# Kernel tuning notes

Hardware: AMD Instinct MI355X
Metric: run time of the kernel (lower is better)

Reference implementation:

```python
import jax, jax.numpy as jnp
import numpy as np

NODES, NFEAT = 128, 256


def setup_inputs() -> dict:
    key = jax.random.key(0)
    k1, k2, k3, k4, k5, k6 = jax.random.split(key, 6)
    B = 512
    x = jax.random.normal(k1, (B, NODES, NFEAT), dtype=jnp.float32)
    adj = jax.random.uniform(k2, (B, NODES, NODES), dtype=jnp.float32)
    # GraphConvolution(nfeat, nfeat): weight [nfeat, nfeat], bias [nfeat]
    s = 1.0 / np.sqrt(NFEAT)
    gcn_w = jax.random.uniform(k3, (NFEAT, NFEAT), minval=-s, maxval=s, dtype=jnp.float32)
    gcn_b = jax.random.uniform(k4, (NFEAT,), minval=-s, maxval=s, dtype=jnp.float32)
    # fc: Linear(nfeat*nodes, nfeat), torch layout [out, in]
    s2 = 1.0 / np.sqrt(NFEAT * NODES)
    fc_w = jax.random.uniform(k5, (NFEAT, NFEAT * NODES), minval=-s2, maxval=s2, dtype=jnp.float32)
    fc_b = jax.random.uniform(k6, (NFEAT,), minval=-s2, maxval=s2, dtype=jnp.float32)
    return {"x": x, "adj": adj, "gcn_w": gcn_w, "gcn_b": gcn_b, "fc_w": fc_w, "fc_b": fc_b}


def reference(x, adj, gcn_w, gcn_b, fc_w, fc_b):
    B = x.shape[0]
    # Per-sample loop GCN fused as batched matmuls:
    # support = X @ W ; out = A @ support + b
    support = jnp.einsum('bnf,fg->bng', x, gcn_w)          # [B, nodes, nfeat]
    mid = jnp.einsum('bnm,bmg->bng', adj, support) + gcn_b  # [B, nodes, nfeat]
    # cat along dim0 then reshape(-1, nfeat*nodes) == per-graph flatten
    flat = mid.reshape(B, NODES * NFEAT)
    output = flat @ fc_w.T + fc_b                           # [B, nfeat]
    useful_input = x[:, 0, :]                               # [B, nfeat]
    return (output, useful_input, output)
```

## Files before the change

### kernel.cpp

```cpp
#include <hip/hip_runtime.h>

#define NODES 128
#define NFEAT 256
#define BATCH 512
#define KTOT  (NODES * NFEAT)
#define SPLIT 128
#define KCH   (KTOT / SPLIT)

typedef __bf16 bf16_t;
typedef bf16_t bf16x8 __attribute__((ext_vector_type(8)));
typedef float  f32x4  __attribute__((ext_vector_type(4)));

#define BK    32
#define LDK   40
#define BK2   64
#define LDK2  72
#define LDM   136
#define TILE  128

__device__ __forceinline__ bf16x8 cvt8(const float4 a, const float4 b) {
    bf16x8 t;
    t[0] = (bf16_t)a.x; t[1] = (bf16_t)a.y; t[2] = (bf16_t)a.z; t[3] = (bf16_t)a.w;
    t[4] = (bf16_t)b.x; t[5] = (bf16_t)b.y; t[6] = (bf16_t)b.z; t[7] = (bf16_t)b.w;
    return t;
}

struct XT { float4 v[4]; };
__device__ __forceinline__ void xload(const float* __restrict__ src, int ld, int k0,
                                      int tid, XT& t) {
#pragma unroll
    for (int i = 0; i < 2; i++) {
        int f = tid + i * 256, r = f >> 2, c = f & 3;
        t.v[2 * i]     = *(const float4*)(src + (size_t)r * ld + k0 + c * 8);
        t.v[2 * i + 1] = *(const float4*)(src + (size_t)r * ld + k0 + c * 8 + 4);
    }
}
__device__ __forceinline__ void xstore(bf16_t* __restrict__ dst, int tid, const XT& t) {
#pragma unroll
    for (int i = 0; i < 2; i++) {
        int f = tid + i * 256, r = f >> 2, c = f & 3;
        *(bf16x8*)(dst + r * LDK + c * 8) = cvt8(t.v[2 * i], t.v[2 * i + 1]);
    }
}

struct XT2 { float4 v[8]; };
__device__ __forceinline__ void xload2(const float* __restrict__ src, int ld, int k0,
                                       int tid, XT2& t) {
#pragma unroll
    for (int i = 0; i < 4; i++) {
        int f = tid + i * 256, r = f >> 3, c = f & 7;
        t.v[2 * i]     = *(const float4*)(src + (size_t)r * ld + k0 + c * 8);
        t.v[2 * i + 1] = *(const float4*)(src + (size_t)r * ld + k0 + c * 8 + 4);
    }
}
__device__ __forceinline__ void xstore2(bf16_t* __restrict__ dst, int tid, const XT2& t) {
#pragma unroll
    for (int i = 0; i < 4; i++) {
        int f = tid + i * 256, r = f >> 3, c = f & 7;
        *(bf16x8*)(dst + r * LDK2 + c * 8) = cvt8(t.v[2 * i], t.v[2 * i + 1]);
    }
}

struct AT2 { bf16x8 v[4]; };
__device__ __forceinline__ void aload2(const bf16_t* __restrict__ src, int ld, int k0,
                                       int tid, AT2& t) {
#pragma unroll
    for (int i = 0; i < 4; i++) {
        int f = tid + i * 256, r = f >> 3, c = f & 7;
        t.v[i] = *(const bf16x8*)(src + (size_t)r * ld + k0 + c * 8);
    }
}
__device__ __forceinline__ void astore2(bf16_t* __restrict__ dst, int tid, const AT2& t) {
#pragma unroll
    for (int i = 0; i < 4; i++) {
        int f = tid + i * 256, r = f >> 3, c = f & 7;
        *(bf16x8*)(dst + r * LDK2 + c * 8) = t.v[i];
    }
}

__global__ __launch_bounds__(256)
void k_wt(const float* __restrict__ w, bf16_t* __restrict__ wT) {
    const int g0 = blockIdx.x * 4;
    const int k  = threadIdx.x;
    const float4 v = *(const float4*)(w + (size_t)k * NFEAT + g0);
    wT[(size_t)(g0 + 0) * NFEAT + k] = (bf16_t)v.x;
    wT[(size_t)(g0 + 1) * NFEAT + k] = (bf16_t)v.y;
    wT[(size_t)(g0 + 2) * NFEAT + k] = (bf16_t)v.z;
    wT[(size_t)(g0 + 3) * NFEAT + k] = (bf16_t)v.w;
}

__global__ __launch_bounds__(256)
void k_init(const float* __restrict__ fc_b, const float* __restrict__ x,
            float* __restrict__ out) {
    const int g = blockIdx.x * 256 + threadIdx.x;
    const int o = g & (NFEAT - 1), b = g >> 8;
    out[g] = fc_b[o];
    out[BATCH * NFEAT + g] = x[(size_t)b * NODES * NFEAT + o];
}

__global__ __launch_bounds__(256)
void k_fin(float* __restrict__ out) {
    const int g = blockIdx.x * 256 + threadIdx.x;
    out[2 * BATCH * NFEAT + g] = out[g];
}

__global__ __launch_bounds__(256, 3)
void k_fused12(const float* __restrict__ x, const float* __restrict__ adj,
               const bf16_t* __restrict__ wT, const float* __restrict__ gcn_b,
               bf16_t* __restrict__ mid) {
    __shared__ __align__(16) bf16_t As[TILE * LDK];
    __shared__ __align__(16) bf16_t Sb[TILE * LDM];
    const int n0  = blockIdx.x * TILE;
    const int b   = blockIdx.y;
    const int tid = threadIdx.x;
    const int lane = tid & 63, w = tid >> 6, wm = w & 1, wn = w >> 1;
    const int l15 = lane & 15, q = lane >> 4;
    const float* xb   = x   + (size_t)b * NODES * NFEAT;
    const float* adjb = adj + (size_t)b * NODES * NODES;

    const bf16_t* wrow[4];
#pragma unroll
    for (int j = 0; j < 4; j++)
        wrow[j] = wT + (size_t)(n0 + wn * 64 + j * 16 + l15) * NFEAT + q * 8;

    f32x4 acc[4][4] = {};
    {
        XT r0, rn, r2;
        xload(xb, NFEAT, 0, tid, r0);
        xload(xb, NFEAT, BK, tid, rn);
        bf16x8 bcur[4], bnxt[4];
#pragma unroll
        for (int j = 0; j < 4; j++) bcur[j] = *(const bf16x8*)(wrow[j]);
        xstore(As, tid, r0);
        __syncthreads();
        for (int k0 = 0; k0 < NFEAT; k0 += BK) {
            const bool in1 = (k0 + BK)  < NFEAT;
            const bool in2 = (k0 + 2*BK) < NFEAT;
            if (in2) xload(xb, NFEAT, k0 + 2*BK, tid, r2);
            const int knc = in1 ? k0 + BK : 0;
#pragma unroll
            for (int j = 0; j < 4; j++) bnxt[j] = *(const bf16x8*)(wrow[j] + knc);
            bf16x8 a[4];
#pragma unroll
            for (int i = 0; i < 4; i++)
                a[i] = *(const bf16x8*)(As + (wm * 64 + i * 16 + l15) * LDK + q * 8);
#pragma unroll
            for (int i = 0; i < 4; i++)
#pragma unroll
                for (int j = 0; j < 4; j++)
                    acc[i][j] = __builtin_amdgcn_mfma_f32_16x16x32_bf16(a[i], bcur[j], acc[i][j], 0, 0, 0);
            __syncthreads();
            if (in1) xstore(As, tid, rn);
            rn = r2;
#pragma unroll
            for (int j = 0; j < 4; j++) bcur[j] = bnxt[j];
            __syncthreads();
        }
    }

    XT a0, a1, a2;
    xload(adjb, NODES, 0, tid, a0);
    xload(adjb, NODES, BK, tid, a1);
#pragma unroll
    for (int i = 0; i < 4; i++)
#pragma unroll
        for (int j = 0; j < 4; j++)
#pragma unroll
            for (int r = 0; r < 4; r++) {
                int m = wm * 64 + i * 16 + q * 4 + r;
                int g = wn * 64 + j * 16 + l15;
                Sb[g * LDM + m] = (bf16_t)acc[i][j][r];
            }
    __syncthreads();
    xstore(As, tid, a0);
    __syncthreads();

    f32x4 acc2[4][4] = {};
    for (int k0 = 0; k0 < NODES; k0 += BK) {
        const bool in1 = (k0 + BK)   < NODES;
        const bool in2 = (k0 + 2*BK) < NODES;
        if (in2) xload(adjb, NODES, k0 + 2*BK, tid, a2);
        bf16x8 a[4], bb[4];
#pragma unroll
        for (int i = 0; i < 4; i++)
            a[i] = *(const bf16x8*)(As + (wm * 64 + i * 16 + l15) * LDK + q * 8);
#pragma unroll
        for (int j = 0; j < 4; j++)
            bb[j] = *(const bf16x8*)(Sb + (wn * 64 + j * 16 + l15) * LDM + k0 + q * 8);
#pragma unroll
        for (int i = 0; i < 4; i++)
#pragma unroll
            for (int j = 0; j < 4; j++)
                acc2[i][j] = __builtin_amdgcn_mfma_f32_16x16x32_bf16(a[i], bb[j], acc2[i][j], 0, 0, 0);
        __syncthreads();
        if (in1) xstore(As, tid, a1);
        a1 = a2;
        __syncthreads();
    }
    bf16_t* outb = mid + (size_t)b * NODES * NFEAT;
#pragma unroll
    for (int j = 0; j < 4; j++) {
        int g = n0 + wn * 64 + j * 16 + l15;
        float bias = gcn_b[g];
#pragma unroll
        for (int i = 0; i < 4; i++)
#pragma unroll
            for (int r = 0; r < 4; r++) {
                int node = wm * 64 + i * 16 + q * 4 + r;
                outb[(size_t)node * NFEAT + g] = (bf16_t)(acc2[i][j][r] + bias);
            }
    }
}

__global__ __launch_bounds__(256, 3)
void k_out(const bf16_t* __restrict__ flat, const float* __restrict__ fcw,
           float* __restrict__ out) {
    __shared__ __align__(16) bf16_t As[TILE * LDK2];
    __shared__ __align__(16) bf16_t Bs[TILE * LDK2];
    const int m0 = blockIdx.x * TILE;
    const int n0 = blockIdx.y * TILE;
    const int kb = blockIdx.z * KCH, kend = kb + KCH;
    const int tid = threadIdx.x;
    const int lane = tid & 63, w = tid >> 6, wm = w & 1, wn = w >> 1;
    const int l15 = lane & 15, q = lane >> 4;
    f32x4 acc[4][4] = {};
    const bf16_t* fa = flat + (size_t)m0 * KTOT;
    const float*  fb = fcw + (size_t)n0 * KTOT;

    AT2 at; aload2(fa, KTOT, kb, tid, at);
    XT2 bt; xload2(fb, KTOT, kb, tid, bt);
    astore2(As, tid, at);
    xstore2(Bs, tid, bt);
    __syncthreads();
    for (int k0 = kb; k0 < kend; k0 += BK2) {
        const int kn = k0 + BK2;
        const bool in = kn < kend;
        AT2 an; XT2 bn;
        if (in) { aload2(fa, KTOT, kn, tid, an); xload2(fb, KTOT, kn, tid, bn); }
#pragma unroll
        for (int kk = 0; kk < BK2; kk += BK) {
            bf16x8 a[4], bbf[4];
#pragma unroll
            for (int i = 0; i < 4; i++)
                a[i] = *(const bf16x8*)(As + (wm * 64 + i * 16 + l15) * LDK2 + kk + q * 8);
#pragma unroll
            for (int j = 0; j < 4; j++)
                bbf[j] = *(const bf16x8*)(Bs + (wn * 64 + j * 16 + l15) * LDK2 + kk + q * 8);
#pragma unroll
            for (int i = 0; i < 4; i++)
#pragma unroll
                for (int j = 0; j < 4; j++)
                    acc[i][j] = __builtin_amdgcn_mfma_f32_16x16x32_bf16(a[i], bbf[j], acc[i][j], 0, 0, 0);
        }
        __syncthreads();
        if (in) { astore2(As, tid, an); xstore2(Bs, tid, bn); }
        __syncthreads();
    }
#pragma unroll
    for (int i = 0; i < 4; i++)
#pragma unroll
        for (int j = 0; j < 4; j++)
#pragma unroll
            for (int r = 0; r < 4; r++) {
                int bt_ = m0 + wm * 64 + i * 16 + q * 4 + r;
                int o   = n0 + wn * 64 + j * 16 + l15;
                atomicAdd(&out[(size_t)bt_ * NFEAT + o], acc[i][j][r]);
            }
}

extern "C" void kernel_launch(void* const* d_in, const int* in_sizes, int n_in,
                              void* d_out, int out_size, void* d_ws, size_t ws_size,
                              hipStream_t stream) {
    const float* x     = (const float*)d_in[0];
    const float* adj   = (const float*)d_in[1];
    const float* gcn_w = (const float*)d_in[2];
    const float* gcn_b = (const float*)d_in[3];
    const float* fc_w  = (const float*)d_in[4];
    const float* fc_b  = (const float*)d_in[5];
    float* out = (float*)d_out;

    bf16_t* wT  = (bf16_t*)d_ws;
    bf16_t* mid = (bf16_t*)((char*)d_ws + 131072);

    k_wt     <<<dim3(64), dim3(256), 0, stream>>>(gcn_w, wT);
    k_init   <<<dim3(BATCH), dim3(256), 0, stream>>>(fc_b, x, out);
    k_fused12<<<dim3(2, BATCH), dim3(256), 0, stream>>>(x, adj, wT, gcn_b, mid);
    k_out    <<<dim3(4, 2, SPLIT), dim3(256), 0, stream>>>(mid, fc_w, out);
    k_fin    <<<dim3(BATCH), dim3(256), 0, stream>>>(out);
}
```

Baseline: 238.9 us.

## Replace split-K atomics with bf16 partials plus reduce kernel; lighter barriers

The split-K output GEMM now writes bf16 partial tiles to workspace instead of float atomics into the output. A new reduce kernel sums them, adds the bias, and writes all three outputs, which removes the init and finish kernels. The split factor is halved to 64, and __syncthreads is replaced by an inline s_waitcnt lgkmcnt(0) plus s_barrier that skips waiting on outstanding global loads. Rounding partials to bf16 adds accumulation error, and the reduce pass adds extra memory traffic.

Measured after the change: 203.7 us. 14.7% less time.

```diff
diff --git a/kernel.cpp b/kernel.cpp
--- a/kernel.cpp
+++ b/kernel.cpp
@@ -4,7 +4,7 @@
 #define NFEAT 256
 #define BATCH 512
 #define KTOT  (NODES * NFEAT)
-#define SPLIT 128
+#define SPLIT 64
 #define KCH   (KTOT / SPLIT)
 
 typedef __bf16 bf16_t;
@@ -17,6 +17,10 @@
 #define LDK2  72
 #define LDM   136
 #define TILE  128
+
+__device__ __forceinline__ void bar() {
+    asm volatile("s_waitcnt lgkmcnt(0)\n\ts_barrier" ::: "memory");
+}
 
 __device__ __forceinline__ bf16x8 cvt8(const float4 a, const float4 b) {
     bf16x8 t;
@@ -87,21 +91,6 @@
     wT[(size_t)(g0 + 1) * NFEAT + k] = (bf16_t)v.y;
     wT[(size_t)(g0 + 2) * NFEAT + k] = (bf16_t)v.z;
     wT[(size_t)(g0 + 3) * NFEAT + k] = (bf16_t)v.w;
-}
-
-__global__ __launch_bounds__(256)
-void k_init(const float* __restrict__ fc_b, const float* __restrict__ x,
-            float* __restrict__ out) {
-    const int g = blockIdx.x * 256 + threadIdx.x;
-    const int o = g & (NFEAT - 1), b = g >> 8;
-    out[g] = fc_b[o];
-    out[BATCH * NFEAT + g] = x[(size_t)b * NODES * NFEAT + o];
-}
-
-__global__ __launch_bounds__(256)
-void k_fin(float* __restrict__ out) {
-    const int g = blockIdx.x * 256 + threadIdx.x;
-    out[2 * BATCH * NFEAT + g] = out[g];
 }
 
 __global__ __launch_bounds__(256, 3)
@@ -132,9 +121,9 @@
 #pragma unroll
         for (int j = 0; j < 4; j++) bcur[j] = *(const bf16x8*)(wrow[j]);
         xstore(As, tid, r0);
-        __syncthreads();
+        bar();
         for (int k0 = 0; k0 < NFEAT; k0 += BK) {
-            const bool in1 = (k0 + BK)  < NFEAT;
+            const bool in1 = (k0 + BK)   < NFEAT;
             const bool in2 = (k0 + 2*BK) < NFEAT;
             if (in2) xload(xb, NFEAT, k0 + 2*BK, tid, r2);
             const int knc = in1 ? k0 + BK : 0;
@@ -149,12 +138,12 @@
 #pragma unroll
                 for (int j = 0; j < 4; j++)
                     acc[i][j] = __builtin_amdgcn_mfma_f32_16x16x32_bf16(a[i], bcur[j], acc[i][j], 0, 0, 0);
-            __syncthreads();
+            bar();
             if (in1) xstore(As, tid, rn);
             rn = r2;
 #pragma unroll
             for (int j = 0; j < 4; j++) bcur[j] = bnxt[j];
-            __syncthreads();
+            bar();
         }
     }
 
@@ -171,9 +160,9 @@
                 int g = wn * 64 + j * 16 + l15;
                 Sb[g * LDM + m] = (bf16_t)acc[i][j][r];
             }
-    __syncthreads();
+    bar();
     xstore(As, tid, a0);
-    __syncthreads();
+    bar();
 
     f32x4 acc2[4][4] = {};
     for (int k0 = 0; k0 < NODES; k0 += BK) {
@@ -192,10 +181,10 @@
 #pragma unroll
             for (int j = 0; j < 4; j++)
                 acc2[i][j] = __builtin_amdgcn_mfma_f32_16x16x32_bf16(a[i], bb[j], acc2[i][j], 0, 0, 0);
-        __syncthreads();
+        bar();
         if (in1) xstore(As, tid, a1);
         a1 = a2;
-        __syncthreads();
+        bar();
     }
     bf16_t* outb = mid + (size_t)b * NODES * NFEAT;
 #pragma unroll
@@ -214,7 +203,7 @@
 
 __global__ __launch_bounds__(256, 3)
 void k_out(const bf16_t* __restrict__ flat, const float* __restrict__ fcw,
-           float* __restrict__ out) {
+           bf16_t* __restrict__ part) {
     __shared__ __align__(16) bf16_t As[TILE * LDK2];
     __shared__ __align__(16) bf16_t Bs[TILE * LDK2];
     const int m0 = blockIdx.x * TILE;
@@ -231,7 +220,7 @@
     XT2 bt; xload2(fb, KTOT, kb, tid, bt);
     astore2(As, tid, at);
     xstore2(Bs, tid, bt);
-    __syncthreads();
+    bar();
     for (int k0 = kb; k0 < kend; k0 += BK2) {
         const int kn = k0 + BK2;
         const bool in = kn < kend;
@@ -252,10 +241,11 @@
                 for (int j = 0; j < 4; j++)
                     acc[i][j] = __builtin_amdgcn_mfma_f32_16x16x32_bf16(a[i], bbf[j], acc[i][j], 0, 0, 0);
         }
-        __syncthreads();
+        bar();
         if (in) { astore2(As, tid, an); xstore2(Bs, tid, bn); }
-        __syncthreads();
-    }
+        bar();
+    }
+    bf16_t* pb = part + (size_t)blockIdx.z * BATCH * NFEAT;
 #pragma unroll
     for (int i = 0; i < 4; i++)
 #pragma unroll
@@ -264,8 +254,36 @@
             for (int r = 0; r < 4; r++) {
                 int bt_ = m0 + wm * 64 + i * 16 + q * 4 + r;
                 int o   = n0 + wn * 64 + j * 16 + l15;
-                atomicAdd(&out[(size_t)bt_ * NFEAT + o], acc[i][j][r]);
+                pb[(size_t)bt_ * NFEAT + o] = (bf16_t)acc[i][j][r];
             }
+}
+
+__global__ __launch_bounds__(256)
+void k_reduce(const bf16_t* __restrict__ part, const float* __restrict__ fc_b,
+              const float* __restrict__ x, float* __restrict__ out) {
+    const int g8 = (blockIdx.x * 256 + threadIdx.x) * 8;
+    const int o = g8 & (NFEAT - 1), b = g8 >> 8;
+    float s[8];
+    const float4 c0 = *(const float4*)(fc_b + o);
+    const float4 c1 = *(const float4*)(fc_b + o + 4);
+    s[0] = c0.x; s[1] = c0.y; s[2] = c0.z; s[3] = c0.w;
+    s[4] = c1.x; s[5] = c1.y; s[6] = c1.z; s[7] = c1.w;
+#pragma unroll 8
+    for (int i = 0; i < SPLIT; i++) {
+        bf16x8 p = *(const bf16x8*)(part + (size_t)i * BATCH * NFEAT + g8);
+#pragma unroll
+        for (int j = 0; j < 8; j++) s[j] += (float)p[j];
+    }
+    float4 o0 = make_float4(s[0], s[1], s[2], s[3]);
+    float4 o1 = make_float4(s[4], s[5], s[6], s[7]);
+    *(float4*)(out + g8)     = o0;
+    *(float4*)(out + g8 + 4) = o1;
+    *(float4*)(out + 2 * BATCH * NFEAT + g8)     = o0;
+    *(float4*)(out + 2 * BATCH * NFEAT + g8 + 4) = o1;
+    const float4 x0 = *(const float4*)(x + (size_t)b * NODES * NFEAT + o);
+    const float4 x1 = *(const float4*)(x + (size_t)b * NODES * NFEAT + o + 4);
+    *(float4*)(out + BATCH * NFEAT + g8)     = x0;
+    *(float4*)(out + BATCH * NFEAT + g8 + 4) = x1;
 }
 
 extern "C" void kernel_launch(void* const* d_in, const int* in_sizes, int n_in,
@@ -279,12 +297,12 @@
     const float* fc_b  = (const float*)d_in[5];
     float* out = (float*)d_out;
 
-    bf16_t* wT  = (bf16_t*)d_ws;
-    bf16_t* mid = (bf16_t*)((char*)d_ws + 131072);
+    bf16_t* wT   = (bf16_t*)d_ws;
+    bf16_t* mid  = (bf16_t*)((char*)d_ws + 131072);
+    bf16_t* part = (bf16_t*)((char*)d_ws + 131072 + (size_t)BATCH * NODES * NFEAT * 2);
 
     k_wt     <<<dim3(64), dim3(256), 0, stream>>>(gcn_w, wT);
-    k_init   <<<dim3(BATCH), dim3(256), 0, stream>>>(fc_b, x, out);
     k_fused12<<<dim3(2, BATCH), dim3(256), 0, stream>>>(x, adj, wT, gcn_b, mid);
-    k_out    <<<dim3(4, 2, SPLIT), dim3(256), 0, stream>>>(mid, fc_w, out);
-    k_fin    <<<dim3(BATCH), dim3(256), 0, stream>>>(out);
-}
+    k_out    <<<dim3(4, 2, SPLIT), dim3(256), 0, stream>>>(mid, fc_w, part);
+    k_reduce <<<dim3(64), dim3(256), 0, stream>>>(part, fc_b, x, out);
+}
```
